# Kernel tuning notes

Measured on AMD Instinct MI355X. Metric: run time of the kernel, lower is better.

Reference implementation:

```python
import jax, jax.numpy as jnp
import numpy as np

B, S = 4, 4096          # batch, tokens (64x64 SAM ViT-H grid)
DIN, DOUT = 1280, 3840  # qkv linear dims
RANK = 16
NUM_SHARED = 1
NUM_ROUTED = 6
TOP_K = 3


def setup_inputs() -> dict:
    key = jax.random.key(0)
    ks = jax.random.split(key, 9)
    s = 0.02
    return {
        "x": jax.random.normal(ks[0], (B, S, DIN), dtype=jnp.float32),
        "base_w": jax.random.normal(ks[1], (DIN, DOUT), dtype=jnp.float32) * s,
        "base_b": jax.random.normal(ks[2], (DOUT,), dtype=jnp.float32) * s,
        "shared_w1": jax.random.normal(ks[3], (NUM_SHARED, DIN, RANK), dtype=jnp.float32) * s,
        "shared_w2": jax.random.normal(ks[4], (NUM_SHARED, RANK, DOUT), dtype=jnp.float32) * s,
        "routed_w1": jax.random.normal(ks[5], (NUM_ROUTED, DIN, RANK), dtype=jnp.float32) * s,
        "routed_w2": jax.random.normal(ks[6], (NUM_ROUTED, RANK, DOUT), dtype=jnp.float32) * s,
        "router_w": jax.random.normal(ks[7], (DIN, NUM_ROUTED), dtype=jnp.float32) * s,
        "router_b": jax.random.normal(ks[8], (NUM_ROUTED,), dtype=jnp.float32) * s,
    }


def reference(x, base_w, base_b, shared_w1, shared_w2, routed_w1, routed_w2, router_w, router_b):
    b, s, din = x.shape
    # base linear runs under torch.no_grad() -> stop_gradient
    base = jax.lax.stop_gradient(jnp.einsum('bsi,io->bso', x, base_w) + base_b)
    # shared low-rank experts, summed over the shared set
    shared = jnp.einsum('bsi,eir,ero->bso', x, shared_w1, shared_w2)
    # router: softmax gates, top-k selection
    gates = jax.nn.softmax(x @ router_w + router_b, axis=-1)      # [B,S,E]
    topk_w, topk_idx = jax.lax.top_k(gates, TOP_K)                # [B,S,K]
    T = b * s
    xf = x.reshape(T, din)
    # combine weights: per-token weight for each expert (top-k indices are
    # distinct, so scatter-add reproduces the per-slot assignment exactly)
    cw = jnp.zeros((T, NUM_ROUTED), dtype=x.dtype).at[
        jnp.arange(T)[:, None], topk_idx.reshape(T, TOP_K)
    ].add(topk_w.reshape(T, TOP_K))                               # [T,E]
    # routed experts: contract rank and expert dims without materializing [T,E,DOUT]
    h = jnp.einsum('ti,eir->ter', xf, routed_w1)                  # [T,E,RANK]
    routed = jnp.einsum('ter,ero,te->to', h, routed_w2, cw).reshape(b, s, DOUT)
    return base + shared + routed
```

## Files before the change

kernel.cpp:

```cpp
#include <hip/hip_runtime.h>
#include <cstdint>
#include <cstddef>

#define DIN 1280
#define DOUT 3840
#define NEXP 6
#define RANK 16
#define TOKENS 16384
#define KPAD 1408
#define NLOW 128

typedef __bf16 bf16x8 __attribute__((ext_vector_type(8)));
typedef float f32x4 __attribute__((ext_vector_type(4)));

__device__ __forceinline__ unsigned short f2bf(float f) {
    unsigned u = __builtin_bit_cast(unsigned, f);
    u += 0x7fff + ((u >> 16) & 1);
    return (unsigned short)(u >> 16);
}

__device__ __forceinline__ void async_load16(void* lds, const void* g) {
    __builtin_amdgcn_global_load_lds(
        (const __attribute__((address_space(1))) unsigned int*)g,
        (__attribute__((address_space(3))) unsigned int*)lds, 16, 0, 0);
}

__global__ void prep_w2t(const float* __restrict__ base_w,
                         const float* __restrict__ shared_w2,
                         const float* __restrict__ routed_w2,
                         unsigned short* __restrict__ WT) {
    __shared__ unsigned short tile[32][33];
    int k0 = blockIdx.x * 32, n0 = blockIdx.y * 32;
    int tx = threadIdx.x, ty = threadIdx.y;
#pragma unroll
    for (int j = 0; j < 4; j++) {
        int k = k0 + ty + j * 8;
        int n = n0 + tx;
        float v;
        if (k < DIN)            v = base_w[(size_t)k * DOUT + n];
        else if (k < DIN + 16)  v = shared_w2[(size_t)(k - DIN) * DOUT + n];
        else if (k < DIN + 112) v = routed_w2[(size_t)(k - DIN - 16) * DOUT + n];
        else                    v = 0.f;
        tile[ty + j * 8][tx] = f2bf(v);
    }
    __syncthreads();
#pragma unroll
    for (int j = 0; j < 4; j++) {
        int n = n0 + ty + j * 8;
        int k = k0 + tx;
        WT[(size_t)n * KPAD + k] = tile[tx][ty + j * 8];
    }
}

__global__ void prep_w1t(const float* __restrict__ shared_w1,
                         const float* __restrict__ routed_w1,
                         unsigned short* __restrict__ W1T) {
    __shared__ unsigned short tile[32][33];
    int k0 = blockIdx.x * 32, n0 = blockIdx.y * 32;
    int tx = threadIdx.x, ty = threadIdx.y;
#pragma unroll
    for (int j = 0; j < 4; j++) {
        int k = k0 + ty + j * 8;
        int n = n0 + tx;
        float v = 0.f;
        if (n < 16) v = shared_w1[k * RANK + n];
        else if (n < 112) {
            int jj = n - 16, e = jj >> 4, r = jj & 15;
            v = routed_w1[(size_t)e * DIN * RANK + k * RANK + r];
        }
        tile[ty + j * 8][tx] = f2bf(v);
    }
    __syncthreads();
#pragma unroll
    for (int j = 0; j < 4; j++) {
        int n = n0 + ty + j * 8;
        int k = k0 + tx;
        W1T[(size_t)n * DIN + k] = tile[tx][ty + j * 8];
    }
}

__global__ __launch_bounds__(256) void router_kernel(
    const float* __restrict__ x,
    const float* __restrict__ router_w,
    const float* __restrict__ router_b,
    unsigned short* __restrict__ A,
    float* __restrict__ cw) {
    int tid = threadIdx.x;
    size_t t0 = (size_t)blockIdx.x * 8;
    const float* xblk = x + t0 * DIN;
    unsigned short* Ablk = A + t0 * KPAD;

    for (int i = tid; i < 8 * DIN; i += 256) {
        int t = i / DIN, c = i - t * DIN;
        Ablk[t * KPAD + c] = f2bf(xblk[i]);
    }
    if (tid < 128) {
        int t = tid >> 4, c = tid & 15;
        Ablk[t * KPAD + DIN + 112 + c] = 0;
    }

    int tg = tid >> 5, lj = tid & 31;
    const float* xt = xblk + (size_t)tg * DIN;
    float acc[6] = {0.f, 0.f, 0.f, 0.f, 0.f, 0.f};
    for (int k = lj; k < DIN; k += 32) {
        float xv = xt[k];
        const float* wr = router_w + k * NEXP;
#pragma unroll
        for (int e = 0; e < NEXP; e++) acc[e] = fmaf(xv, wr[e], acc[e]);
    }
#pragma unroll
    for (int off = 16; off > 0; off >>= 1)
#pragma unroll
        for (int e = 0; e < NEXP; e++) acc[e] += __shfl_xor(acc[e], off);

    float mx = -1e30f;
#pragma unroll
    for (int e = 0; e < NEXP; e++) { acc[e] += router_b[e]; mx = fmaxf(mx, acc[e]); }
    float g[6]; float s = 0.f;
#pragma unroll
    for (int e = 0; e < NEXP; e++) { g[e] = __expf(acc[e] - mx); s += g[e]; }
    float inv = 1.f / s;
    if (lj < NEXP) {
        float ge = g[lj];
        int cnt = 0;
#pragma unroll
        for (int e = 0; e < NEXP; e++) {
            if (e == lj) continue;
            if (g[e] > ge || (g[e] == ge && e < lj)) cnt++;
        }
        cw[(t0 + tg) * NEXP + lj] = (cnt < 3) ? ge * inv : 0.f;
    }
}

__global__ __launch_bounds__(256) void combine_kernel(
    const float* __restrict__ H, const float* __restrict__ cw,
    unsigned short* __restrict__ A) {
    int i = blockIdx.x * 256 + threadIdx.x;
    int t = i / 112, j = i - t * 112;
    float h = H[(size_t)t * NLOW + j];
    float f = (j < 16) ? 1.0f : cw[t * NEXP + ((j - 16) >> 4)];
    A[(size_t)t * KPAD + DIN + j] = f2bf(f * h);
}

template <bool ADD_BIAS>
__global__ __launch_bounds__(256, 2) void gemm_bt(
    const unsigned short* __restrict__ A,
    const unsigned short* __restrict__ BT,
    const float* __restrict__ bias,
    float* __restrict__ C,
    int N, int K, int lda) {
    __shared__ unsigned short ldsA[128 * 32];
    __shared__ unsigned short ldsB[128 * 32];
    int tid = threadIdx.x;
    int lane = tid & 63, wave = tid >> 6;
    int m0 = blockIdx.y * 128, n0 = blockIdx.x * 128;
    int wm = (wave >> 1) * 64, wn = (wave & 1) * 64;
    int lr = lane & 15, quad = lane >> 4;

    f32x4 acc[4][4] = {};

    const unsigned short* Abase = A + (size_t)m0 * lda;
    const unsigned short* Bbase = BT + (size_t)n0 * K;

    for (int k0 = 0; k0 < K; k0 += 32) {
#pragma unroll
        for (int i = 0; i < 2; i++) {
            int c = i * 256 + tid;
            int row = c >> 2;
            int col = (c & 3) << 3;
            async_load16(&ldsA[(i * 256 + wave * 64) * 8],
                         Abase + (size_t)row * lda + k0 + col);
            async_load16(&ldsB[(i * 256 + wave * 64) * 8],
                         Bbase + (size_t)row * K + k0 + col);
        }
        __syncthreads();
        bf16x8 af[4], bf[4];
#pragma unroll
        for (int mi = 0; mi < 4; mi++)
            af[mi] = *(const bf16x8*)&ldsA[(wm + mi * 16 + lr) * 32 + quad * 8];
#pragma unroll
        for (int ni = 0; ni < 4; ni++)
            bf[ni] = *(const bf16x8*)&ldsB[(wn + ni * 16 + lr) * 32 + quad * 8];
#pragma unroll
        for (int mi = 0; mi < 4; mi++)
#pragma unroll
            for (int ni = 0; ni < 4; ni++)
                acc[mi][ni] = __builtin_amdgcn_mfma_f32_16x16x32_bf16(
                    af[mi], bf[ni], acc[mi][ni], 0, 0, 0);
        __syncthreads();
    }

#pragma unroll
    for (int ni = 0; ni < 4; ni++) {
        int gn = n0 + wn + ni * 16 + lr;
        float bv = ADD_BIAS ? bias[gn] : 0.0f;
#pragma unroll
        for (int mi = 0; mi < 4; mi++) {
            int gm = m0 + wm + mi * 16 + quad * 4;
            f32x4 v = acc[mi][ni];
#pragma unroll
            for (int r = 0; r < 4; r++)
                C[(size_t)(gm + r) * N + gn] = v[r] + bv;
        }
    }
}

extern "C" void kernel_launch(void* const* d_in, const int* in_sizes, int n_in,
                              void* d_out, int out_size, void* d_ws, size_t ws_size,
                              hipStream_t stream) {
    const float* x         = (const float*)d_in[0];
    const float* base_w    = (const float*)d_in[1];
    const float* base_b    = (const float*)d_in[2];
    const float* shared_w1 = (const float*)d_in[3];
    const float* shared_w2 = (const float*)d_in[4];
    const float* routed_w1 = (const float*)d_in[5];
    const float* routed_w2 = (const float*)d_in[6];
    const float* router_w  = (const float*)d_in[7];
    const float* router_b  = (const float*)d_in[8];
    float* out = (float*)d_out;

    char* ws = (char*)d_ws;
    size_t off = 0;
    unsigned short* A     = (unsigned short*)(ws + off); off += (size_t)TOKENS * KPAD * 2;
    unsigned short* WcatT = (unsigned short*)(ws + off); off += (size_t)DOUT * KPAD * 2;
    unsigned short* W1T   = (unsigned short*)(ws + off); off += (size_t)NLOW * DIN * 2;
    float* H              = (float*)(ws + off);          off += (size_t)TOKENS * NLOW * 4;
    float* cw             = (float*)(ws + off);          off += (size_t)TOKENS * NEXP * 4;

    prep_w2t<<<dim3(KPAD / 32, DOUT / 32), dim3(32, 8), 0, stream>>>(
        base_w, shared_w2, routed_w2, WcatT);
    prep_w1t<<<dim3(DIN / 32, NLOW / 32), dim3(32, 8), 0, stream>>>(
        shared_w1, routed_w1, W1T);
    router_kernel<<<TOKENS / 8, 256, 0, stream>>>(x, router_w, router_b, A, cw);
    gemm_bt<false><<<dim3(NLOW / 128, TOKENS / 128), 256, 0, stream>>>(
        A, W1T, nullptr, H, NLOW, DIN, KPAD);
    combine_kernel<<<(TOKENS * 112) / 256, 256, 0, stream>>>(H, cw, A);
    gemm_bt<true><<<dim3(DOUT / 128, TOKENS / 128), 256, 0, stream>>>(
        A, WcatT, base_b, out, DOUT, KPAD, KPAD);
}
```

Measured before the change: 353.2 us.

## Replace main GEMM with pipelined 256x256 tile kernel and split-K low-rank GEMM

The main bf16 GEMM now uses a 256x256 tile with 512 threads, double-buffered LDS with XOR swizzling, explicit waitcnt/barrier scheduling, setprio around MFMA groups and XCD-aware block mapping. The aim is more data reuse per tile, overlap of global loads with MFMA work, and fewer LDS bank conflicts. The small rank-projection GEMM is split along K into two halves that write separate partial buffers, and the combine kernel sums them, which doubles the block count for that skinny GEMM. The router's x-to-bf16 conversion is vectorised to 8 elements per thread. The trade-off is heavier LDS use and register pressure, hand-tuned scheduling that is fragile, and an extra partial-sum buffer.

```diff
diff --git a/kernel.cpp b/kernel.cpp
--- a/kernel.cpp
+++ b/kernel.cpp
@@ -12,6 +12,10 @@
 
 typedef __bf16 bf16x8 __attribute__((ext_vector_type(8)));
 typedef float f32x4 __attribute__((ext_vector_type(4)));
+typedef unsigned short u16x8 __attribute__((ext_vector_type(8)));
+
+#define SB() __builtin_amdgcn_sched_barrier(0)
+#define BAR() __builtin_amdgcn_s_barrier()
 
 __device__ __forceinline__ unsigned short f2bf(float f) {
     unsigned u = __builtin_bit_cast(unsigned, f);
@@ -90,9 +94,15 @@
     const float* xblk = x + t0 * DIN;
     unsigned short* Ablk = A + t0 * KPAD;
 
-    for (int i = tid; i < 8 * DIN; i += 256) {
-        int t = i / DIN, c = i - t * DIN;
-        Ablk[t * KPAD + c] = f2bf(xblk[i]);
+    for (int i = tid; i < 8 * (DIN / 8); i += 256) {
+        int t = i / (DIN / 8), c = (i - t * (DIN / 8)) * 8;
+        const float* xs = xblk + (size_t)t * DIN + c;
+        f32x4 v0 = *(const f32x4*)xs;
+        f32x4 v1 = *(const f32x4*)(xs + 4);
+        u16x8 o;
+#pragma unroll
+        for (int j = 0; j < 4; j++) { o[j] = f2bf(v0[j]); o[4 + j] = f2bf(v1[j]); }
+        *(u16x8*)&Ablk[(size_t)t * KPAD + c] = o;
     }
     if (tid < 128) {
         int t = tid >> 4, c = tid & 15;
@@ -137,41 +147,40 @@
     unsigned short* __restrict__ A) {
     int i = blockIdx.x * 256 + threadIdx.x;
     int t = i / 112, j = i - t * 112;
-    float h = H[(size_t)t * NLOW + j];
+    float h = H[(size_t)t * NLOW + j] + H[(size_t)TOKENS * NLOW + (size_t)t * NLOW + j];
     float f = (j < 16) ? 1.0f : cw[t * NEXP + ((j - 16) >> 4)];
     A[(size_t)t * KPAD + DIN + j] = f2bf(f * h);
 }
 
-template <bool ADD_BIAS>
-__global__ __launch_bounds__(256, 2) void gemm_bt(
+__global__ __launch_bounds__(256, 2) void gemm_small(
     const unsigned short* __restrict__ A,
     const unsigned short* __restrict__ BT,
-    const float* __restrict__ bias,
-    float* __restrict__ C,
-    int N, int K, int lda) {
+    float* __restrict__ H) {
     __shared__ unsigned short ldsA[128 * 32];
     __shared__ unsigned short ldsB[128 * 32];
+    const int KS = DIN / 2;
     int tid = threadIdx.x;
     int lane = tid & 63, wave = tid >> 6;
-    int m0 = blockIdx.y * 128, n0 = blockIdx.x * 128;
+    int m0 = blockIdx.y * 128;
+    int z = blockIdx.z;
     int wm = (wave >> 1) * 64, wn = (wave & 1) * 64;
     int lr = lane & 15, quad = lane >> 4;
 
     f32x4 acc[4][4] = {};
-
-    const unsigned short* Abase = A + (size_t)m0 * lda;
-    const unsigned short* Bbase = BT + (size_t)n0 * K;
-
-    for (int k0 = 0; k0 < K; k0 += 32) {
+    const unsigned short* Abase = A + (size_t)m0 * KPAD + z * KS;
+    const unsigned short* Bbase = BT + z * KS;
+    float* Cbase = H + (size_t)z * TOKENS * NLOW;
+
+    for (int k0 = 0; k0 < KS; k0 += 32) {
 #pragma unroll
         for (int i = 0; i < 2; i++) {
             int c = i * 256 + tid;
             int row = c >> 2;
             int col = (c & 3) << 3;
             async_load16(&ldsA[(i * 256 + wave * 64) * 8],
-                         Abase + (size_t)row * lda + k0 + col);
+                         Abase + (size_t)row * KPAD + k0 + col);
             async_load16(&ldsB[(i * 256 + wave * 64) * 8],
-                         Bbase + (size_t)row * K + k0 + col);
+                         Bbase + (size_t)row * DIN + k0 + col);
         }
         __syncthreads();
         bf16x8 af[4], bf[4];
@@ -189,18 +198,141 @@
                     af[mi], bf[ni], acc[mi][ni], 0, 0, 0);
         __syncthreads();
     }
-
 #pragma unroll
     for (int ni = 0; ni < 4; ni++) {
-        int gn = n0 + wn + ni * 16 + lr;
-        float bv = ADD_BIAS ? bias[gn] : 0.0f;
+        int gn = wn + ni * 16 + lr;
 #pragma unroll
         for (int mi = 0; mi < 4; mi++) {
             int gm = m0 + wm + mi * 16 + quad * 4;
             f32x4 v = acc[mi][ni];
 #pragma unroll
             for (int r = 0; r < 4; r++)
-                C[(size_t)(gm + r) * N + gn] = v[r] + bv;
+                Cbase[(size_t)(gm + r) * NLOW + gn] = v[r];
+        }
+    }
+}
+
+
+#define READ_AQ(AQ, MB) do { \
+    AQ[0][0] = rdA(a_cur, (MB) + 0, 0); AQ[0][1] = rdA(a_cur, (MB) + 0, 1); \
+    AQ[1][0] = rdA(a_cur, (MB) + 1, 0); AQ[1][1] = rdA(a_cur, (MB) + 1, 1); \
+} while (0)
+
+#define MFMA_QUAD(AQ, MB) do { \
+    _Pragma("unroll") for (int ks_ = 0; ks_ < 2; ks_++) \
+    _Pragma("unroll") for (int mq_ = 0; mq_ < 2; mq_++) \
+    _Pragma("unroll") for (int ni_ = 0; ni_ < 4; ni_++) \
+        acc[(MB) + mq_][ni_] = __builtin_amdgcn_mfma_f32_16x16x32_bf16( \
+            AQ[mq_][ks_], bfr[ni_][ks_], acc[(MB) + mq_][ni_], 0, 0, 0); \
+} while (0)
+
+__global__ __launch_bounds__(512, 2) void gemm256(
+    const unsigned short* __restrict__ A,
+    const unsigned short* __restrict__ BT,
+    const float* __restrict__ bias,
+    float* __restrict__ C) {
+    __shared__ unsigned short lA[2][256 * 64];
+    __shared__ unsigned short lB[2][256 * 64];
+
+    int tid = threadIdx.x;
+    int lane = tid & 63, wave = tid >> 6;
+    int bid = blockIdx.x;
+    int xcd = bid & 7, lid = bid >> 3;
+    int mt = xcd * 8 + (lid & 7);
+    int nt = lid >> 3;
+    int m0 = mt * 256, n0 = nt * 256;
+
+    int wm = (wave >> 2) * 128, wn = (wave & 3) * 64;
+    int lr = lane & 15, quad = lane >> 4;
+    int swz = (lr & 7) << 4;
+
+    int sr = lane >> 3;
+    int sc = (lane & 7) ^ sr;
+    const unsigned short* aSrc = A + (size_t)(m0 + wave * 32 + sr) * KPAD + sc * 8;
+    const unsigned short* bSrc = BT + (size_t)(n0 + wave * 32 + sr) * KPAD + sc * 8;
+
+    auto stA4 = [&](unsigned short* dst, int k0) {
+#pragma unroll
+        for (int i = 0; i < 4; i++)
+            async_load16(dst + (size_t)(wave * 32 + i * 8) * 64,
+                         aSrc + (size_t)(i * 8) * KPAD + k0);
+    };
+    auto stB1 = [&](unsigned short* dst, int k0, int i) {
+        async_load16(dst + (size_t)(wave * 32 + i * 8) * 64,
+                     bSrc + (size_t)(i * 8) * KPAD + k0);
+    };
+    auto rdA = [&](const unsigned short* base, int mi, int ks) -> bf16x8 {
+        int row = wm + mi * 16 + lr;
+        int off = row * 128 + (((ks << 6) | (quad << 4)) ^ swz);
+        return *(const bf16x8*)((const char*)base + off);
+    };
+    auto rdB = [&](const unsigned short* base, int ni, int ks) -> bf16x8 {
+        int row = wn + ni * 16 + lr;
+        int off = row * 128 + (((ks << 6) | (quad << 4)) ^ swz);
+        return *(const bf16x8*)((const char*)base + off);
+    };
+
+    f32x4 acc[8][4] = {};
+
+    stA4(&lA[0][0], 0);
+#pragma unroll
+    for (int i = 0; i < 4; i++) stB1(&lB[0][0], 0, i);
+#pragma unroll
+    for (int i = 0; i < 4; i++) stB1(&lB[1][0], 64, i);
+    asm volatile("s_waitcnt vmcnt(4)" ::: "memory");
+    SB(); BAR(); SB();
+
+    const int nkt = KPAD / 64;
+#pragma unroll 2
+    for (int t = 0; t < nkt; ++t) {
+        const int ct = t & 1;
+        unsigned short* a_cur = &lA[ct][0];
+        unsigned short* b_cur = &lB[ct][0];
+        unsigned short* a_nxt = &lA[ct ^ 1][0];
+        int k0 = t * 64;
+
+        bf16x8 bfr[4][2];
+#pragma unroll
+        for (int ni = 0; ni < 4; ni++) {
+            bfr[ni][0] = rdB(b_cur, ni, 0);
+            bfr[ni][1] = rdB(b_cur, ni, 1);
+        }
+        SB();
+        bf16x8 aq0[2][2], aq1[2][2], aq2[2][2], aq3[2][2];
+        READ_AQ(aq0, 0);
+        READ_AQ(aq1, 2);
+        if (t + 1 < nkt) stA4(a_nxt, k0 + 64);
+
+        READ_AQ(aq2, 4);
+        __builtin_amdgcn_s_setprio(1); MFMA_QUAD(aq0, 0); __builtin_amdgcn_s_setprio(0);
+        asm volatile("s_waitcnt lgkmcnt(8)" ::: "memory");
+        SB(); BAR(); SB();
+
+        READ_AQ(aq3, 6);
+        if (t + 2 < nkt) { stB1(b_cur, k0 + 128, 0); stB1(b_cur, k0 + 128, 1); }
+        __builtin_amdgcn_s_setprio(1); MFMA_QUAD(aq1, 2); __builtin_amdgcn_s_setprio(0);
+
+        if (t + 2 < nkt) { stB1(b_cur, k0 + 128, 2); stB1(b_cur, k0 + 128, 3); }
+        __builtin_amdgcn_s_setprio(1); MFMA_QUAD(aq2, 4); __builtin_amdgcn_s_setprio(0);
+
+        __builtin_amdgcn_s_setprio(1); MFMA_QUAD(aq3, 6); __builtin_amdgcn_s_setprio(0);
+
+        if (t + 2 < nkt) asm volatile("s_waitcnt vmcnt(4) lgkmcnt(0)" ::: "memory");
+        else             asm volatile("s_waitcnt vmcnt(0) lgkmcnt(0)" ::: "memory");
+        SB(); BAR(); SB();
+    }
+
+#pragma unroll
+    for (int mi = 0; mi < 8; mi++) {
+        int gm = m0 + wm + mi * 16 + quad * 4;
+#pragma unroll
+        for (int ni = 0; ni < 4; ni++) {
+            int gn = n0 + wn + ni * 16 + lr;
+            float bv = bias[gn];
+            f32x4 v = acc[mi][ni];
+#pragma unroll
+            for (int r = 0; r < 4; r++)
+                C[(size_t)(gm + r) * DOUT + gn] = v[r] + bv;
         }
     }
 }
@@ -224,7 +356,7 @@
     unsigned short* A     = (unsigned short*)(ws + off); off += (size_t)TOKENS * KPAD * 2;
     unsigned short* WcatT = (unsigned short*)(ws + off); off += (size_t)DOUT * KPAD * 2;
     unsigned short* W1T   = (unsigned short*)(ws + off); off += (size_t)NLOW * DIN * 2;
-    float* H              = (float*)(ws + off);          off += (size_t)TOKENS * NLOW * 4;
+    float* H              = (float*)(ws + off);          off += (size_t)2 * TOKENS * NLOW * 4;
     float* cw             = (float*)(ws + off);          off += (size_t)TOKENS * NEXP * 4;
 
     prep_w2t<<<dim3(KPAD / 32, DOUT / 32), dim3(32, 8), 0, stream>>>(
@@ -232,9 +364,7 @@
     prep_w1t<<<dim3(DIN / 32, NLOW / 32), dim3(32, 8), 0, stream>>>(
         shared_w1, routed_w1, W1T);
     router_kernel<<<TOKENS / 8, 256, 0, stream>>>(x, router_w, router_b, A, cw);
-    gemm_bt<false><<<dim3(NLOW / 128, TOKENS / 128), 256, 0, stream>>>(
-        A, W1T, nullptr, H, NLOW, DIN, KPAD);
+    gemm_small<<<dim3(1, TOKENS / 128, 2), 256, 0, stream>>>(A, W1T, H);
     combine_kernel<<<(TOKENS * 112) / 256, 256, 0, stream>>>(H, cw, A);
-    gemm_bt<true><<<dim3(DOUT / 128, TOKENS / 128), 256, 0, stream>>>(
-        A, WcatT, base_b, out, DOUT, KPAD, KPAD);
-}
+    gemm256<<<(TOKENS / 256) * (DOUT / 256), 512, 0, stream>>>(A, WcatT, base_b, out);
+}
```

After: 284.9 us. 19.3% less time.
